# Kernel optimization log

Measured on AMD Instinct MI355X. Metric: run time of the kernel, lower is better.

## Reference

```python
import jax, jax.numpy as jnp
import numpy as np

B, S, F, D = 4, 1024, 8, 512
H = 8
DK = D // H
DF = 2048
ECLIPSE_BOOST = 2.0
LN_EPS = 1e-5


def _layer_norm(x, g, b):
    m = jnp.mean(x, axis=-1, keepdims=True)
    v = jnp.mean(jnp.square(x - m), axis=-1, keepdims=True)
    return (x - m) * jax.lax.rsqrt(v + LN_EPS) * g + b


def setup_inputs() -> dict:
    key = jax.random.key(0)
    ks = jax.random.split(key, 16)
    def lin_w(k, out_d, in_d):
        return jax.random.normal(k, (out_d, in_d), jnp.float32) * (1.0 / np.sqrt(in_d))
    return {
        "x": jax.random.normal(ks[0], (B, S, F, D), jnp.float32),
        "eclipse_mask": jax.random.bernoulli(ks[1], 0.3, (B, S)),
        "wq": lin_w(ks[2], D, D), "bq": jnp.zeros((D,), jnp.float32),
        "wk": lin_w(ks[3], D, D), "bk": jnp.zeros((D,), jnp.float32),
        "wv": lin_w(ks[4], D, D), "bv": jnp.zeros((D,), jnp.float32),
        "wo": lin_w(ks[5], D, D), "bo": jnp.zeros((D,), jnp.float32),
        "w1": lin_w(ks[6], DF, D), "b1": jnp.zeros((DF,), jnp.float32),
        "w2": lin_w(ks[7], D, DF), "b2": jnp.zeros((D,), jnp.float32),
        "g1": jnp.ones((D,), jnp.float32), "be1": jnp.zeros((D,), jnp.float32),
        "g2": jnp.ones((D,), jnp.float32), "be2": jnp.zeros((D,), jnp.float32),
    }


def reference(x, eclipse_mask, wq, bq, wk, bk, wv, bv, wo, bo, w1, b1, w2, b2, g1, be1, g2, be2):
    BF = B * F
    scale = 1.0 / np.sqrt(DK)
    # NOTE: the torch module does x.view(B*F, S, D) on a [B,S,F,D] tensor —
    # a raw memory reshape (NOT a transpose). Replicate exactly.
    xr = x.reshape(BF, S, D)  # [BF, S, D]
    # eclipse_mask [B,S] -> expand over features -> [BF, S] (rows b*F+f share mask[b])
    em = jnp.broadcast_to(eclipse_mask[:, None, :], (B, F, S)).reshape(BF, S)

    def proj(w, b):
        return (xr @ w.T + b).reshape(BF, S, H, DK).transpose(0, 2, 1, 3)  # [BF,H,S,DK]

    Q, K, V = proj(wq, bq), proj(wk, bk), proj(wv, bv)
    scores = jnp.einsum("bhqd,bhkd->bhqk", Q, K) * scale  # [BF,H,S,S]
    boost = jnp.where(em, ECLIPSE_BOOST, 1.0)[:, None, None, :]  # over key positions
    scores = scores * boost
    attn = jax.nn.softmax(scores, axis=-1)
    ctx = jnp.einsum("bhqk,bhkd->bhqd", attn, V)  # [BF,H,S,DK]
    ctx = ctx.transpose(0, 2, 1, 3).reshape(BF, S, D)
    attn_out = (ctx @ wo.T + bo).reshape(B, S, F, D)  # raw reshape back, matches torch

    h = _layer_norm(x + attn_out, g1, be1)
    ff = jax.nn.gelu(h @ w1.T + b1, approximate=False) @ w2.T + b2
    return _layer_norm(h + ff, g2, be2)
```

## Files before the change

### kernel.cpp

```cpp
#include <hip/hip_runtime.h>
#include <math.h>

typedef _Float16 half8 __attribute__((ext_vector_type(8)));
typedef float f32x4 __attribute__((ext_vector_type(4)));
typedef float f32x16 __attribute__((ext_vector_type(16)));
typedef unsigned int u32;

#define AS1 __attribute__((address_space(1)))
#define AS3 __attribute__((address_space(3)))

__device__ __forceinline__ void g2lds16(const void* g, void* l) {
    __builtin_amdgcn_global_load_lds((const AS1 u32*)g, (AS3 u32*)l, 16, 0, 0);
}

#if __has_builtin(__builtin_amdgcn_exp2f)
#define EXP2F(x) __builtin_amdgcn_exp2f(x)
#else
#define EXP2F(x) exp2f(x)
#endif

__device__ __forceinline__ u32 pk2(float a, float b) {
    auto h2 = __builtin_amdgcn_cvt_pkrtz(a, b);
    return __builtin_bit_cast(u32, h2);
}
__device__ __forceinline__ half8 mkh8(u32 a, u32 b, u32 c, u32 d) {
    union { half8 h; u32 u[4]; } x;
    x.u[0] = a; x.u[1] = b; x.u[2] = c; x.u[3] = d;
    return x.h;
}

#define MFMA32(a, b, c) __builtin_amdgcn_mfma_f32_32x32x16_f16(a, b, c, 0, 0, 0)

__global__ __launch_bounds__(256)
void cvt_all(const float* __restrict__ x, const float* __restrict__ wq,
             const float* __restrict__ wk, const float* __restrict__ wv,
             const float* __restrict__ wo, const float* __restrict__ w1,
             const float* __restrict__ w2, _Float16* __restrict__ xh,
             _Float16* __restrict__ qkvw, _Float16* __restrict__ woh,
             _Float16* __restrict__ w1h, _Float16* __restrict__ w2h)
{
    const int bid = blockIdx.x;
    const float* src; _Float16* dst; int g;
    if (bid < 8192)      { src = x;  dst = xh;            g = bid*256 + threadIdx.x; }
    else if (bid < 8320) { src = wq; dst = qkvw;          g = (bid-8192)*256 + threadIdx.x; }
    else if (bid < 8448) { src = wk; dst = qkvw + 262144; g = (bid-8320)*256 + threadIdx.x; }
    else if (bid < 8576) { src = wv; dst = qkvw + 524288; g = (bid-8448)*256 + threadIdx.x; }
    else if (bid < 8704) { src = wo; dst = woh;           g = (bid-8576)*256 + threadIdx.x; }
    else if (bid < 9216) { src = w1; dst = w1h;           g = (bid-8704)*256 + threadIdx.x; }
    else                 { src = w2; dst = w2h;           g = (bid-9216)*256 + threadIdx.x; }
    const float4* p = (const float4*)src + (size_t)g * 2;
    float4 a = p[0], b = p[1];
    half8 h;
    h[0]=(_Float16)a.x; h[1]=(_Float16)a.y; h[2]=(_Float16)a.z; h[3]=(_Float16)a.w;
    h[4]=(_Float16)b.x; h[5]=(_Float16)b.y; h[6]=(_Float16)b.z; h[7]=(_Float16)b.w;
    *((half8*)dst + g) = h;
}

__global__ __launch_bounds__(256)
void pack_bias(const float* __restrict__ bq, const float* __restrict__ bk,
               const float* __restrict__ bv, float* __restrict__ o)
{
    const int i = blockIdx.x * 256 + threadIdx.x;
    o[i] = i < 512 ? bq[i] : (i < 1024 ? bk[i-512] : bv[i-1024]);
}

template<int MODE>
__global__ __launch_bounds__(256)
void gemm_bt(const _Float16* __restrict__ A, const _Float16* __restrict__ B,
             const float* __restrict__ bias, const float* __restrict__ resf,
             const _Float16* __restrict__ resh, const int* __restrict__ emask,
             _Float16* __restrict__ vTout, void* __restrict__ Cout,
             int M, int N, int K)
{
    __shared__ __align__(16) _Float16 As[128 * 32];
    __shared__ __align__(16) _Float16 Bs[128 * 32];
    __shared__ __align__(16) _Float16 Ts[(MODE == 0) ? 128 * 132 : 4];
    const int tid = threadIdx.x;
    const int lane = tid & 63;
    const int w = tid >> 6;
    const int wm = w >> 1, wn = w & 1;

    const int gx = gridDim.x;
    const int nwg = gx * gridDim.y;
    int bid = blockIdx.y * gx + blockIdx.x;
    bid = (bid & 7) * (nwg >> 3) + (bid >> 3);
    const int m0 = (bid / gx) * 128, n0 = (bid % gx) * 128;

    const int lrow = lane & 15;
    const int lk = (lane >> 4) * 8;

    f32x4 acc[4][4];
#pragma unroll
    for (int i = 0; i < 4; ++i)
#pragma unroll
        for (int j = 0; j < 4; ++j) acc[i][j] = (f32x4)0.0f;

    for (int k0 = 0; k0 < K; k0 += 32) {
#pragma unroll
        for (int i = 0; i < 2; ++i) {
            int gbase = i * 256 + w * 64;
            int g = gbase + lane;
            g2lds16(A + (size_t)(m0 + (g >> 2)) * K + k0 + (g & 3) * 8,
                    (char*)As + (size_t)gbase * 16);
            g2lds16(B + (size_t)(n0 + (g >> 2)) * K + k0 + (g & 3) * 8,
                    (char*)Bs + (size_t)gbase * 16);
        }
        __syncthreads();
        half8 af[4], bfr[4];
#pragma unroll
        for (int t = 0; t < 4; ++t) {
            af[t]  = *(const half8*)(As + (wm * 64 + t * 16 + lrow) * 32 + lk);
            bfr[t] = *(const half8*)(Bs + (wn * 64 + t * 16 + lrow) * 32 + lk);
        }
#pragma unroll
        for (int mi = 0; mi < 4; ++mi)
#pragma unroll
            for (int ni = 0; ni < 4; ++ni)
                acc[mi][ni] = __builtin_amdgcn_mfma_f32_16x16x32_f16(af[mi], bfr[ni], acc[mi][ni], 0, 0, 0);
        __syncthreads();
    }

    const int rq = (lane >> 4) * 4;

    if (MODE == 0 && n0 >= 1024) {
#pragma unroll
        for (int mi = 0; mi < 4; ++mi) {
#pragma unroll
            for (int ni = 0; ni < 4; ++ni) {
                const int coll = wn * 64 + ni * 16 + lrow;
                const float bv = bias[n0 + coll];
                const int rowb = wm * 64 + mi * 16 + rq;
                uint2 pkd;
                pkd.x = pk2(acc[mi][ni][0] + bv, acc[mi][ni][1] + bv);
                pkd.y = pk2(acc[mi][ni][2] + bv, acc[mi][ni][3] + bv);
                *(uint2*)&Ts[coll * 132 + rowb] = pkd;
            }
        }
        __syncthreads();
        const int l31 = lane & 31, lh = lane >> 5;
        const int bf_ = m0 >> 10;
        const int sb  = m0 & 1023;
        const int sl  = 4 * l31;
        const int posl = (sl & ~12) | ((sl & 4) << 1) | ((sl & 8) >> 1);
#pragma unroll
        for (int it = 0; it < 16; ++it) {
            const int dkl = w * 32 + it * 2 + lh;
            uint2 val = *(const uint2*)&Ts[dkl * 132 + sl];
            const int dkf = (n0 - 1024) + dkl;
            _Float16* dst = vTout + (((size_t)(bf_ * 8 + (dkf >> 6))) << 16)
                          + ((size_t)(dkf & 63) << 10) + sb + posl;
            *(uint2*)dst = val;
        }
        return;
    }

#pragma unroll
    for (int mi = 0; mi < 4; ++mi) {
        float bst[4];
        if (MODE == 0 && n0 >= 512) {
#pragma unroll
            for (int r = 0; r < 4; ++r) {
                const int row = m0 + wm * 64 + mi * 16 + rq + r;
                bst[r] = emask[((row >> 13) << 10) | (row & 1023)] ? 2.0f : 1.0f;
            }
        }
#pragma unroll
        for (int ni = 0; ni < 4; ++ni) {
            const int col = n0 + wn * 64 + ni * 16 + lrow;
            const float bv = bias[col];
#pragma unroll
            for (int r = 0; r < 4; ++r) {
                const int row = m0 + wm * 64 + mi * 16 + rq + r;
                const size_t idx = (size_t)row * N + col;
                float v = acc[mi][ni][r] + bv;
                if (MODE == 0) {
                    ((_Float16*)Cout)[idx] = (_Float16)(n0 >= 512 ? v * bst[r] : v);
                } else if (MODE == 1) {
                    float t2 = -1.5957691216057308f * v * fmaf(v * v, 0.044715f, 1.0f);
                    float e = __expf(t2);
                    ((_Float16*)Cout)[idx] = (_Float16)(v * __builtin_amdgcn_rcpf(1.0f + e));
                } else if (MODE == 2) {
                    ((float*)Cout)[idx] = v + resf[idx];
                } else {
                    ((float*)Cout)[idx] = v + (float)resh[idx];
                }
            }
        }
    }
}

__global__ __launch_bounds__(256, 3)
void attn_fwd(const _Float16* __restrict__ QKV, const _Float16* __restrict__ vT,
              _Float16* __restrict__ ctx)
{
    __shared__ __align__(16) char KsB[2][8192];
    __shared__ __align__(16) char VsB[2][8192];
    __shared__ float den[4][32];
    __shared__ char occ_pad[8192];

    const int tid = threadIdx.x;
    const int lane = tid & 63;
    const int w = tid >> 6;
    if (tid == 0xFFFFu) occ_pad[0] = 1;

    const int p = blockIdx.y * 8 + blockIdx.x;
    const int ii = p >> 3;
    const int headlin = (p & 7) * 32 + (ii >> 3);
    const int bf = headlin >> 3;
    const int hh = headlin & 7;
    const int q0 = (ii & 7) * 128;

    const int l31 = lane & 31;
    const int hi = lane >> 5;

    constexpr float SC = 0.18033688f;
    constexpr float B2 = -7.2134752f;

    half8 qf[4];
    {
        const _Float16* qp = QKV + (size_t)(bf * 1024 + q0 + w * 32 + l31) * 1536 + hh * 64 + hi * 8;
        qf[0] = *(const half8*)qp;
        qf[1] = *(const half8*)(qp + 16);
        qf[2] = *(const half8*)(qp + 32);
        qf[3] = *(const half8*)(qp + 48);
    }

    const char* Kg = (const char*)(QKV + (size_t)bf * 1536 * 1024 + 512 + hh * 64);
    const char* Vg = (const char*)(vT + (size_t)(bf * 8 + hh) * 65536);

    f32x16 acc0 = (f32x16)0.f, acc1 = (f32x16)0.f;
    float dsum = 0.f;

    const int rsub = lane >> 3;
    const int boff = ((lane & 7) * 16) ^ (rsub << 4);

#define STAGE(Kd, Vd, ktn)                                                         \
    {                                                                              \
        _Pragma("unroll")                                                          \
        for (int j = 0; j < 2; ++j) {                                              \
            const int row_ = w * 16 + j * 8 + rsub;                                \
            g2lds16(Kg + (size_t)((ktn) + row_) * 3072 + boff,                     \
                    (Kd) + w * 2048 + j * 1024);                                   \
            g2lds16(Vg + (size_t)row_ * 2048 + (ktn) * 2 + boff,                   \
                    (Vd) + w * 2048 + j * 1024);                                   \
        }                                                                          \
    }

    STAGE(KsB[0], VsB[0], 0);
    __syncthreads();

    const int kx = (l31 & 7) << 4;

    for (int kt = 0; kt < 1024; kt += 64) {
        const int cur = (kt >> 6) & 1;
        const char* Kb = KsB[cur];
        const char* Vb = VsB[cur];
        STAGE(KsB[cur ^ 1], VsB[cur ^ 1], (kt + 64) & 1023);

#pragma unroll
        for (int t = 0; t < 2; ++t) {
            const int kb = (t * 32 + l31) * 128 + hi * 16;
            half8 kf0 = *(const half8*)(Kb + ((kb      ) ^ kx));
            half8 kf1 = *(const half8*)(Kb + ((kb +  32) ^ kx));
            half8 kf2 = *(const half8*)(Kb + ((kb +  64) ^ kx));
            half8 kf3 = *(const half8*)(Kb + ((kb +  96) ^ kx));

            f32x16 s = (f32x16)0.f;
            s = MFMA32(kf0, qf[0], s); s = MFMA32(kf1, qf[1], s);
            s = MFMA32(kf2, qf[2], s); s = MFMA32(kf3, qf[3], s);

            float e0 = EXP2F(fmaf(s[0],  SC, B2)),  e1 = EXP2F(fmaf(s[1],  SC, B2));
            float e2 = EXP2F(fmaf(s[2],  SC, B2)),  e3 = EXP2F(fmaf(s[3],  SC, B2));
            float e4 = EXP2F(fmaf(s[4],  SC, B2)),  e5 = EXP2F(fmaf(s[5],  SC, B2));
            float e6 = EXP2F(fmaf(s[6],  SC, B2)),  e7 = EXP2F(fmaf(s[7],  SC, B2));
            float e8 = EXP2F(fmaf(s[8],  SC, B2)),  e9 = EXP2F(fmaf(s[9],  SC, B2));
            float e10 = EXP2F(fmaf(s[10], SC, B2)), e11 = EXP2F(fmaf(s[11], SC, B2));
            float e12 = EXP2F(fmaf(s[12], SC, B2)), e13 = EXP2F(fmaf(s[13], SC, B2));
            float e14 = EXP2F(fmaf(s[14], SC, B2)), e15 = EXP2F(fmaf(s[15], SC, B2));
            dsum += (((e0+e1)+(e2+e3)) + ((e4+e5)+(e6+e7)))
                  + (((e8+e9)+(e10+e11)) + ((e12+e13)+(e14+e15)));
            half8 pa0 = mkh8(pk2(e0, e1), pk2(e2, e3), pk2(e4, e5), pk2(e6, e7));
            half8 pa1 = mkh8(pk2(e8, e9), pk2(e10, e11), pk2(e12, e13), pk2(e14, e15));

            {
                const int vb = l31 * 128 + t * 64 + hi * 16;
                half8 vfs0 = *(const half8*)(Vb + ((vb     ) ^ kx));
                half8 vfs1 = *(const half8*)(Vb + ((vb + 32) ^ kx));
                acc0 = MFMA32(pa0, vfs0, acc0);
                acc0 = MFMA32(pa1, vfs1, acc0);
            }
            {
                const int vb = (32 + l31) * 128 + t * 64 + hi * 16;
                half8 vfs0 = *(const half8*)(Vb + ((vb     ) ^ kx));
                half8 vfs1 = *(const half8*)(Vb + ((vb + 32) ^ kx));
                acc1 = MFMA32(pa0, vfs0, acc1);
                acc1 = MFMA32(pa1, vfs1, acc1);
            }
        }
        __syncthreads();
    }

    dsum += __shfl_xor(dsum, 32);
    den[w][l31] = dsum;
    __syncthreads();

#pragma unroll
    for (int r = 0; r < 16; ++r) {
        const int crow = (r & 3) + 8 * (r >> 2) + 4 * hi;
        const float inv = 1.0f / den[w][crow];
        const int qrow = q0 + w * 32 + crow;
        _Float16* cp = ctx + ((size_t)bf * 1024 + qrow) * 512 + hh * 64 + l31;
        cp[0]  = (_Float16)(acc0[r] * inv);
        cp[32] = (_Float16)(acc1[r] * inv);
    }
#undef STAGE
}

template<int OUTH>
__global__ __launch_bounds__(256)
void ln_fused(const float* __restrict__ X, const float* __restrict__ gma,
              const float* __restrict__ bta, float* __restrict__ outF,
              _Float16* __restrict__ outH)
{
    const int row = blockIdx.x * 4 + (threadIdx.x >> 6);
    const int lane = threadIdx.x & 63;
    const float4* xr = (const float4*)(X + (size_t)row * 512);
    float4 a = xr[lane * 2], c = xr[lane * 2 + 1];
    float s  = a.x + a.y + a.z + a.w + c.x + c.y + c.z + c.w;
    float s2 = a.x * a.x + a.y * a.y + a.z * a.z + a.w * a.w
             + c.x * c.x + c.y * c.y + c.z * c.z + c.w * c.w;
#pragma unroll
    for (int m = 1; m < 64; m <<= 1) { s += __shfl_xor(s, m); s2 += __shfl_xor(s2, m); }
    const float mean = s * (1.0f / 512.0f);
    const float inv = rsqrtf(s2 * (1.0f / 512.0f) - mean * mean + 1e-5f);
    const float4* gp = (const float4*)gma;
    const float4* bp = (const float4*)bta;
    float4 g0 = gp[lane * 2], g1 = gp[lane * 2 + 1];
    float4 b0 = bp[lane * 2], b1 = bp[lane * 2 + 1];
    float4 o0, o1;
    o0.x = (a.x - mean) * inv * g0.x + b0.x; o0.y = (a.y - mean) * inv * g0.y + b0.y;
    o0.z = (a.z - mean) * inv * g0.z + b0.z; o0.w = (a.w - mean) * inv * g0.w + b0.w;
    o1.x = (c.x - mean) * inv * g1.x + b1.x; o1.y = (c.y - mean) * inv * g1.y + b1.y;
    o1.z = (c.z - mean) * inv * g1.z + b1.z; o1.w = (c.w - mean) * inv * g1.w + b1.w;
    if (OUTH) {
        half8 hv;
        hv[0] = (_Float16)o0.x; hv[1] = (_Float16)o0.y; hv[2] = (_Float16)o0.z; hv[3] = (_Float16)o0.w;
        hv[4] = (_Float16)o1.x; hv[5] = (_Float16)o1.y; hv[6] = (_Float16)o1.z; hv[7] = (_Float16)o1.w;
        *((half8*)(outH + (size_t)row * 512) + lane) = hv;
    } else {
        float4* op = (float4*)(outF + (size_t)row * 512);
        op[lane * 2] = o0; op[lane * 2 + 1] = o1;
    }
}

extern "C" void kernel_launch(void* const* d_in, const int* in_sizes, int n_in,
                              void* d_out, int out_size, void* d_ws, size_t ws_size,
                              hipStream_t stream)
{
    const float* x   = (const float*)d_in[0];
    const int* mask  = (const int*)d_in[1];
    const float* wq  = (const float*)d_in[2];  const float* bq  = (const float*)d_in[3];
    const float* wk  = (const float*)d_in[4];  const float* bk  = (const float*)d_in[5];
    const float* wv  = (const float*)d_in[6];  const float* bv  = (const float*)d_in[7];
    const float* wo  = (const float*)d_in[8];  const float* bo  = (const float*)d_in[9];
    const float* w1  = (const float*)d_in[10]; const float* b1  = (const float*)d_in[11];
    const float* w2  = (const float*)d_in[12]; const float* b2  = (const float*)d_in[13];
    const float* g1  = (const float*)d_in[14]; const float* be1 = (const float*)d_in[15];
    const float* g2  = (const float*)d_in[16]; const float* be2 = (const float*)d_in[17];
    float* out = (float*)d_out;

    char* ws = (char*)d_ws;
    _Float16* qkvh = (_Float16*)(ws);
    _Float16* ctxh = (_Float16*)(ws + 100663296);
    _Float16* gh   = (_Float16*)(ws);
    _Float16* xh   = (_Float16*)(ws + 134217728);
    float*    res  = (float*)   (ws + 134217728);
    _Float16* vTh  = (_Float16*)(ws + 167772160);
    _Float16* hhb  = (_Float16*)(ws + 201326592);
    float*    biasf= (float*)   (ws + 201326592);
    _Float16* qkvw = (_Float16*)(ws + 234881024);
    _Float16* woh  = (_Float16*)(ws + 236453888);
    _Float16* w1h  = (_Float16*)(ws + 236978176);
    _Float16* w2h  = (_Float16*)(ws + 239075328);

    dim3 blk(256);

    cvt_all<<<9728, blk, 0, stream>>>(x, wq, wk, wv, wo, w1, w2, xh, qkvw, woh, w1h, w2h);
    pack_bias<<<6, blk, 0, stream>>>(bq, bk, bv, biasf);

    gemm_bt<0><<<dim3(12, 256), blk, 0, stream>>>(xh, qkvw, biasf, nullptr, nullptr, mask, vTh, qkvh, 32768, 1536, 512);

    attn_fwd<<<dim3(8, 256), blk, 0, stream>>>(qkvh, vTh, ctxh);

    gemm_bt<2><<<dim3(4, 256), blk, 0, stream>>>(ctxh, woh, bo, x, nullptr, nullptr, nullptr, res, 32768, 512, 512);

    ln_fused<1><<<8192, blk, 0, stream>>>(res, g1, be1, nullptr, hhb);

    gemm_bt<1><<<dim3(16, 256), blk, 0, stream>>>(hhb, w1h, b1, nullptr, nullptr, nullptr, nullptr, gh, 32768, 2048, 512);

    gemm_bt<3><<<dim3(4, 256), blk, 0, stream>>>(gh, w2h, b2, nullptr, hhb, nullptr, nullptr, res, 32768, 512, 2048);

    ln_fused<0><<<8192, blk, 0, stream>>>(res, g2, be2, out, nullptr);
}
```

Before: 660.9 us.

## Double-buffer GEMM LDS tiles with swizzle and use exp2-based GELU

The GEMM main loop now prefetches the next K tile into a second LDS buffer while MFMAs consume the current one, so there is one barrier per iteration instead of two. The LDS chunk layout is XOR-swizzled to reduce bank conflicts on fragment reads, and the transpose buffer aliases the same shared memory. The GELU epilogue folds log2(e) into its constants so it can use exp2 directly. LDS use per block doubles, which may reduce occupancy.

```diff
diff --git a/kernel.cpp b/kernel.cpp
--- a/kernel.cpp
+++ b/kernel.cpp
@@ -72,9 +72,11 @@
              _Float16* __restrict__ vTout, void* __restrict__ Cout,
              int M, int N, int K)
 {
-    __shared__ __align__(16) _Float16 As[128 * 32];
-    __shared__ __align__(16) _Float16 Bs[128 * 32];
-    __shared__ __align__(16) _Float16 Ts[(MODE == 0) ? 128 * 132 : 4];
+    __shared__ __align__(16) char smem[(MODE == 0) ? 33792 : 32768];
+    char* Asb = smem;
+    char* Bsb = smem + 16384;
+    _Float16* Ts = (_Float16*)smem;
+
     const int tid = threadIdx.x;
     const int lane = tid & 63;
     const int w = tid >> 6;
@@ -87,7 +89,7 @@
     const int m0 = (bid / gx) * 128, n0 = (bid % gx) * 128;
 
     const int lrow = lane & 15;
-    const int lk = (lane >> 4) * 8;
+    const int q = lane >> 4;
 
     f32x4 acc[4][4];
 #pragma unroll
@@ -95,29 +97,47 @@
 #pragma unroll
         for (int j = 0; j < 4; ++j) acc[i][j] = (f32x4)0.0f;
 
+#define GSTAGE(curb, k0v)                                                        \
+    {                                                                            \
+        _Pragma("unroll")                                                        \
+        for (int i = 0; i < 2; ++i) {                                            \
+            const int gbase = i * 256 + w * 64;                                  \
+            const int g = gbase + lane;                                          \
+            const int row = g >> 2, s = g & 3;                                   \
+            const int chunk = s ^ ((row >> 1) & 3);                              \
+            g2lds16(A + (size_t)(m0 + row) * K + (k0v) + chunk * 8,              \
+                    Asb + (curb) * 8192 + gbase * 16);                           \
+            g2lds16(B + (size_t)(n0 + row) * K + (k0v) + chunk * 8,              \
+                    Bsb + (curb) * 8192 + gbase * 16);                           \
+        }                                                                        \
+    }
+
+    GSTAGE(0, 0);
+    __syncthreads();
+
+    const int swz = ((lrow >> 1) & 3) << 4;
+    int cur = 0;
+
     for (int k0 = 0; k0 < K; k0 += 32) {
-#pragma unroll
-        for (int i = 0; i < 2; ++i) {
-            int gbase = i * 256 + w * 64;
-            int g = gbase + lane;
-            g2lds16(A + (size_t)(m0 + (g >> 2)) * K + k0 + (g & 3) * 8,
-                    (char*)As + (size_t)gbase * 16);
-            g2lds16(B + (size_t)(n0 + (g >> 2)) * K + k0 + (g & 3) * 8,
-                    (char*)Bs + (size_t)gbase * 16);
-        }
-        __syncthreads();
+        if (k0 + 32 < K) GSTAGE(cur ^ 1, k0 + 32);
+
         half8 af[4], bfr[4];
 #pragma unroll
         for (int t = 0; t < 4; ++t) {
-            af[t]  = *(const half8*)(As + (wm * 64 + t * 16 + lrow) * 32 + lk);
-            bfr[t] = *(const half8*)(Bs + (wn * 64 + t * 16 + lrow) * 32 + lk);
+            const int ar = wm * 64 + t * 16 + lrow;
+            const int br = wn * 64 + t * 16 + lrow;
+            const int c = (q * 16) ^ swz;
+            af[t]  = *(const half8*)(Asb + cur * 8192 + ar * 64 + c);
+            bfr[t] = *(const half8*)(Bsb + cur * 8192 + br * 64 + c);
         }
 #pragma unroll
         for (int mi = 0; mi < 4; ++mi)
 #pragma unroll
             for (int ni = 0; ni < 4; ++ni)
                 acc[mi][ni] = __builtin_amdgcn_mfma_f32_16x16x32_f16(af[mi], bfr[ni], acc[mi][ni], 0, 0, 0);
+
         __syncthreads();
+        cur ^= 1;
     }
 
     const int rq = (lane >> 4) * 4;
@@ -176,8 +196,8 @@
                 if (MODE == 0) {
                     ((_Float16*)Cout)[idx] = (_Float16)(n0 >= 512 ? v * bst[r] : v);
                 } else if (MODE == 1) {
-                    float t2 = -1.5957691216057308f * v * fmaf(v * v, 0.044715f, 1.0f);
-                    float e = __expf(t2);
+                    float u = v * fmaf(v * v, -0.10294604f, -2.3022079f);
+                    float e = EXP2F(u);
                     ((_Float16*)Cout)[idx] = (_Float16)(v * __builtin_amdgcn_rcpf(1.0f + e));
                 } else if (MODE == 2) {
                     ((float*)Cout)[idx] = v + resf[idx];
@@ -187,6 +207,7 @@
             }
         }
     }
+#undef GSTAGE
 }
 
 __global__ __launch_bounds__(256, 3)
```

After: 615.9 us. 1.07x faster.
